# Optimization experiments

Measured on AMD Instinct MI355X. Metric: run time of the kernel, lower is better.

The kernel has to match this reference:

```python
import jax, jax.numpy as jnp
import numpy as np
from jax import lax

# config (mirrors KeypointExtract init)
NMS_DIST = 4
CONF_THRESH = 0.015
CELL = 8
BORDER = 4
KPT_NUM = 1024
WINDOW_SIZE = 5
TEMP_INIT = 10.0
MAX_CAND = 8192  # fixed candidate budget (top-scoring pixels fed to greedy NMS)


def _make_offsets():
    # linspace(-(ws//2), ws//2, ws//2*2+1) meshgrid -> (R,2) integer offsets (dy, dx)
    lin = np.linspace(-(WINDOW_SIZE // 2), WINDOW_SIZE // 2, num=WINDOW_SIZE // 2 * 2 + 1)
    o0, o1 = np.meshgrid(lin, lin)
    off = np.concatenate([o0.reshape(-1, 1), o1.reshape(-1, 1)], axis=1)
    return jnp.asarray(off.astype(np.int32))  # (R,2)


def depth2space(semi):
    # softmax over 65 channels, drop dustbin, pixel-shuffle 8x8 cells to full res
    dense = jax.nn.softmax(semi, axis=1)
    nodust = dense[:, :-1, :, :]                      # (B,64,Hc,Wc)
    B, C, Hc, Wc = nodust.shape
    cell = CELL
    hm = nodust.transpose(0, 2, 3, 1).reshape(B, Hc, Wc, cell, cell)
    hm = hm.transpose(0, 1, 3, 2, 4).reshape(B, Hc * cell, Wc * cell)
    return hm                                         # (B,H,W)


def greedy_nms(ys, xs, valid, H, W, pad):
    # faithful greedy grid-suppression NMS: candidates arrive sorted by conf desc
    w = 2 * pad + 1
    grid0 = jnp.zeros((H + 2 * pad, W + 2 * pad), dtype=bool)  # True = suppressed

    def step(grid, inp):
        y, x, v = inp
        keep = v & jnp.logical_not(grid[y + pad, x + pad])
        patch = lax.dynamic_slice(grid, (y, x), (w, w))
        grid = lax.dynamic_update_slice(grid, jnp.logical_or(patch, keep), (y, x))
        return grid, keep

    _, kept = lax.scan(step, grid0, (ys, xs, valid))
    return kept


def grid_sample_bilinear(img, gx, gy):
    # torch F.grid_sample, mode=bilinear, padding=zeros, align_corners=False
    B, C, Hc, Wc = img.shape
    ix = (gx + 1.0) * (Wc / 2.0) - 0.5
    iy = (gy + 1.0) * (Hc / 2.0) - 0.5
    x0 = jnp.floor(ix); y0 = jnp.floor(iy)
    wx1 = ix - x0; wy1 = iy - y0
    bidx = jnp.arange(B)[:, None]

    def tap(xi, yi):
        inb = (xi >= 0) & (xi < Wc) & (yi >= 0) & (yi < Hc)
        xc = jnp.clip(xi, 0, Wc - 1).astype(jnp.int32)
        yc = jnp.clip(yi, 0, Hc - 1).astype(jnp.int32)
        v = img[bidx, :, yc, xc]                      # (B,N,C)
        return jnp.where(inb[..., None], v, 0.0)

    v00 = tap(x0, y0); v01 = tap(x0 + 1, y0)
    v10 = tap(x0, y0 + 1); v11 = tap(x0 + 1, y0 + 1)
    w00 = ((1 - wx1) * (1 - wy1))[..., None]
    w01 = (wx1 * (1 - wy1))[..., None]
    w10 = ((1 - wx1) * wy1)[..., None]
    w11 = (wx1 * wy1)[..., None]
    out = v00 * w00 + v01 * w01 + v10 * w10 + v11 * w11  # (B,N,C)
    return out.transpose(0, 2, 1)                        # (B,C,N)


def setup_inputs() -> dict:
    key = jax.random.key(0)
    k1, k2 = jax.random.split(key)
    semi = jax.random.normal(k1, (4, 65, 120, 160), dtype=jnp.float32)
    coarse_desc = jax.random.normal(k2, (4, 256, 120, 160), dtype=jnp.float32)
    temp = jnp.ones((1,), dtype=jnp.float32) * TEMP_INIT
    return {"semi": semi, "coarse_desc": coarse_desc, "temp": temp}


def reference(semi, coarse_desc, temp):
    heatmap = depth2space(semi)                       # (B,H,W)
    B, H, W = heatmap.shape
    offs = _make_offsets()                            # (R,2) = (dy,dx)
    R = offs.shape[0]

    # ---- keypoint detection (no-grad in original) ----
    hm_sg = lax.stop_gradient(heatmap)
    vals, idx = lax.top_k(hm_sg.reshape(B, -1), MAX_CAND)   # sorted conf desc
    ys = (idx // W).astype(jnp.int32)
    xs = (idx % W).astype(jnp.int32)
    valid = vals >= CONF_THRESH
    kept = jax.vmap(lambda y, x, v: greedy_nms(y, x, v, H, W, NMS_DIST))(ys, xs, valid)
    border_ok = (xs >= BORDER) & (xs < W - BORDER) & (ys >= BORDER) & (ys < H - BORDER)
    sel_key = jnp.where(kept & border_ok, vals, -jnp.inf)
    _, sel = lax.top_k(sel_key, KPT_NUM)              # top kpt_num survivors by conf
    ysel = jnp.take_along_axis(ys, sel, axis=1)       # (B,N)
    xsel = jnp.take_along_axis(xs, sel, axis=1)

    # ---- spatial soft-argmax (differentiable) ----
    yy = ysel[:, None, :] + offs[None, :, 0:1]        # (B,R,N)
    xx = xsel[:, None, :] + offs[None, :, 1:2]
    bidx = jnp.arange(B)[:, None, None]
    region = heatmap[bidx, yy, xx]                    # (B,R,N) gather
    attn = jax.nn.softmax(region * temp[0], axis=1)
    offs_f = offs.astype(jnp.float32)
    dy = jnp.einsum('brn,r->bn', attn, offs_f[:, 0])
    dx = jnp.einsum('brn,r->bn', attn, offs_f[:, 1])
    y_f = ysel.astype(jnp.float32) + dy
    x_f = xsel.astype(jnp.float32) + dx
    batch_pts = jnp.stack([x_f, y_f], axis=-1)        # (B,N,2) (x,y)

    # ---- descriptor sampling ----
    gx = x_f / (W / 2.0) - 1.0
    gy = y_f / (H / 2.0) - 1.0
    desc = grid_sample_bilinear(coarse_desc, gx, gy)  # (B,C,N)
    desc = desc / jnp.maximum(jnp.linalg.norm(desc, axis=1, keepdims=True), 1e-12)
    return batch_pts, desc, heatmap
```

## Files before the change

kernel.cpp:

```cpp
#include <hip/hip_runtime.h>
#include <cstdint>

typedef unsigned int u32;
typedef unsigned long long u64;
typedef unsigned short u16;
typedef unsigned char u8;

#define HM_H 960
#define HM_W 1280
#define HM_N (HM_H*HM_W)
#define BATCH 4
#define CAND 8192
#define KPT 1024
#define NCELL 19200

#define WS_HISTA 0x0
#define WS_HISTB 0x100000
#define WS_META  0x200000
#define WS_CAND  0x200400
#define WS_EQ    0x240400
#define WS_SIDX  0x260400
#define WS_SEL   0x280400
#define WS_CM    0x284400
#define WS_CS    0x2CF400
#define WS_SPOT  0x365400
#define WS_BST   0x385400
#define WS_BLST  0x398040
#define WS_CNT   0x3A8040
#define WS_STAT  0x3C8040
#define WS_CLST  0x3D0040
#define WS_CAND2 0x4D0040


#define HBIN0 0x3C75u
#define NHBIN 780

__device__ inline double pixval64(const float* __restrict__ semi, const float* __restrict__ cm,
                                  const double* __restrict__ cs, int b, u32 idx){
  u32 y = idx / HM_W, x = idx - y*HM_W;
  u32 hc = y>>3, wc = x>>3, ch = ((y&7)<<3) | (x&7);
  float logit = semi[(((size_t)b*65 + ch)*120 + hc)*160 + wc];
  int cid = b*NCELL + (int)(hc*160 + wc);
  return exp((double)logit - (double)cm[cid]) / cs[cid];
}

__global__ __launch_bounds__(256) void k_heatmap(const float* __restrict__ semi, float* __restrict__ hm,
                          float* __restrict__ cm, double* __restrict__ cs, u32* __restrict__ hist){
  __shared__ u32 lh[NHBIN];
  for (int i=threadIdx.x;i<NHBIN;i+=256) lh[i]=0;
  __syncthreads();
  const u32 FLOOR = 0x3C75C28Fu;
  int tid = blockIdx.x*256 + threadIdx.x;
  int cell = tid >> 3, sub = tid & 7;
  int wc = cell % 160; int hc = (cell/160) % 120; int b = cell / NCELL;
  const float* p = semi + (size_t)b*65*NCELL + hc*160 + wc;
  float r[8];
  #pragma unroll
  for (int i=0;i<8;i++) r[i] = p[(size_t)(sub*8+i)*NCELL];
  float extra = (sub==7) ? p[(size_t)64*NCELL] : -3.0e38f;
  float m = extra;
  #pragma unroll
  for (int i=0;i<8;i++) m = fmaxf(m, r[i]);
  m = fmaxf(m, __shfl_xor(m,1,64));
  m = fmaxf(m, __shfl_xor(m,2,64));
  m = fmaxf(m, __shfl_xor(m,4,64));
  double S = 0.0;
  #pragma unroll
  for (int i=0;i<8;i++) S += exp((double)r[i] - (double)m);
  if (sub==7) S += exp((double)extra - (double)m);
  S += __shfl_xor(S,1,64);
  S += __shfl_xor(S,2,64);
  S += __shfl_xor(S,4,64);
  if (sub==0){ cm[cell]=m; cs[cell]=S; }
  float* out = hm + ((size_t)b*HM_H + hc*8 + sub)*HM_W + wc*8;
  float o[8];
  #pragma unroll
  for (int i=0;i<8;i++) o[i] = (float)(exp((double)r[i] - (double)m) / S);
  *reinterpret_cast<float4*>(out)     = make_float4(o[0],o[1],o[2],o[3]);
  *reinterpret_cast<float4*>(out + 4) = make_float4(o[4],o[5],o[6],o[7]);
  #pragma unroll
  for (int i=0;i<8;i++){
    u32 bs = __float_as_uint(o[i]);
    if (bs>=FLOOR){ u32 bi=(bs>>16)-HBIN0; if(bi>=NHBIN)bi=NHBIN-1; atomicAdd(&lh[bi],1u); }
  }
  __syncthreads();
  u32* h = hist + b*65536 + HBIN0;
  for (int i=threadIdx.x;i<NHBIN;i+=256){
    u32 c=lh[i]; if (c) atomicAdd(&h[i], c);
  }
}

__global__ __launch_bounds__(256) void k_histB(const float* __restrict__ hm, const u32* __restrict__ meta,
                                               u32* __restrict__ hist){
  const u32 FLOOR = 0x3C75C28Fu;
  int b = blockIdx.x >> 8;
  int chunk = blockIdx.x & 255;
  u32 piv = meta[b*64+0];
  u32* h = hist + b*65536;
  const float4* src = (const float4*)(hm + (size_t)b*HM_N);
  int per = (HM_N/4)/256;
  int start = chunk*per;
  for (int i=start+(int)threadIdx.x; i<start+per; i+=256){
    float4 v = src[i];
    u32 bs;
    bs = __float_as_uint(v.x); if (bs >= FLOOR && (bs>>16)==piv) atomicAdd(&h[bs & 0xFFFFu], 1u);
    bs = __float_as_uint(v.y); if (bs >= FLOOR && (bs>>16)==piv) atomicAdd(&h[bs & 0xFFFFu], 1u);
    bs = __float_as_uint(v.z); if (bs >= FLOOR && (bs>>16)==piv) atomicAdd(&h[bs & 0xFFFFu], 1u);
    bs = __float_as_uint(v.w); if (bs >= FLOOR && (bs>>16)==piv) atomicAdd(&h[bs & 0xFFFFu], 1u);
  }
}

__global__ void k_reduce(const u32* __restrict__ hist, u32* __restrict__ meta, int phase){
  int b = blockIdx.x;
  const u32* h = hist + b*65536;
  u32* mb = meta + b*64;
  u32 K = (phase==0) ? (u32)CAND : mb[1];
  int t = threadIdx.x;
  __shared__ u32 suf[1024];
  u32 s = 0;
  for (int i=0;i<64;i++) s += h[t*64+i];
  suf[t]=s; __syncthreads();
  for (int off=1; off<1024; off<<=1){
    u32 add = (t+off<1024) ? suf[t+off] : 0u;
    u32 nv2 = suf[t] + add;
    __syncthreads();
    suf[t]=nv2; __syncthreads();
  }
  u32 total = suf[0];
  u32 cumAbove = (t<1023) ? suf[t+1] : 0u;
  bool found = (cumAbove < K) && (cumAbove + s >= K);
  if (found){
    u32 cum = cumAbove; int bin = 0; u32 cA = cumAbove;
    for (int i=63;i>=0;i--){
      u32 c = h[t*64+i];
      if (cum + c >= K){ bin = t*64+i; cA = cum; break; }
      cum += c;
    }
    if (phase==0){ mb[0]=(u32)bin; mb[2]=cA; mb[1]=K-cA; }
    else {
      u32 V = (mb[0]<<16) | (u32)bin; mb[3]=V;
      u32 cg = mb[2] + cA; mb[4]=cg;
      mb[5] = (cg < (u32)CAND) ? ((u32)CAND - cg) : 0u;
    }
  }
  if (t==0 && total < K){
    if (phase==0){ mb[0]=0; mb[2]=total; mb[1]=K-total; }
    else {
      u32 V = (mb[0]<<16); mb[3]=V;
      u32 cg = mb[2] + total; mb[4]=cg;
      mb[5] = (cg < (u32)CAND) ? ((u32)CAND - cg) : 0u;
    }
  }
}

#define CB_CAP 4800
__global__ __launch_bounds__(256) void k_compact(const float* __restrict__ hm, u32* __restrict__ meta,
                          u64* __restrict__ cand, u32* __restrict__ eq){
  __shared__ u32 pixb[CB_CAP];
  __shared__ u32 bsb[CB_CAP];
  __shared__ u32 eqb[CB_CAP];
  __shared__ u32 cnt, ecnt, gbase, ebase;
  int b = blockIdx.x >> 8;
  int chunk = blockIdx.x & 255;
  if (threadIdx.x==0){ cnt=0u; ecnt=0u; }
  __syncthreads();
  u32 V = meta[b*64+3];
  const float4* src = (const float4*)(hm + (size_t)b*HM_N);
  int per = (HM_N/4)/256;
  int start = chunk*per;
  for (int i=start+(int)threadIdx.x; i<start+per; i+=256){
    float4 v = src[i];
    u32 pix = (u32)i*4u;
    u32 bs4[4];
    bs4[0]=__float_as_uint(v.x); bs4[1]=__float_as_uint(v.y);
    bs4[2]=__float_as_uint(v.z); bs4[3]=__float_as_uint(v.w);
    #pragma unroll
    for (int c2=0;c2<4;c2++){
      u32 bs = bs4[c2];
      if (bs > V){ u32 p = atomicAdd(&cnt,1u); pixb[p]=pix+(u32)c2; bsb[p]=bs; }
      else if (bs == V){ u32 e = atomicAdd(&ecnt,1u); eqb[e]=pix+(u32)c2; }
    }
  }
  __syncthreads();
  if (threadIdx.x==0){
    gbase = cnt  ? atomicAdd(&meta[b*64+6], cnt)  : 0u;
    ebase = ecnt ? atomicAdd(&meta[b*64+7], ecnt) : 0u;
  }
  __syncthreads();
  u32 c0=cnt, e0=ecnt, gb=gbase, eb=ebase;
  for (u32 i=threadIdx.x; i<c0; i+=256){
    u32 s2 = gb+i;
    if (s2 < CAND) cand[(size_t)b*CAND+s2] = (((u64)(~bsb[i]))<<32)|(u64)pixb[i];
  }
  for (u32 i=threadIdx.x; i<e0; i+=256){
    u32 s2 = eb+i;
    if (s2 < CAND) eq[(size_t)b*CAND+s2] = eqb[i];
  }
}

__global__ void k_eqprep(const u32* __restrict__ meta, u64* __restrict__ cand, const u32* __restrict__ eq,
                         const float* __restrict__ semi, const float* __restrict__ cm,
                         const double* __restrict__ cs){
  int b = blockIdx.x;
  __shared__ double vv[64];
  __shared__ u32 ii[64];
  if (threadIdx.x != 0) return;
  const u32* mb = meta + b*64;
  u32 countGt = mb[4], needEq = mb[5], V32 = mb[3];
  int n = (int)mb[7]; if (n > 64) n = 64;
  for (int j=0;j<n;j++){
    ii[j] = eq[(size_t)b*CAND + j];
    vv[j] = pixval64(semi, cm, cs, b, ii[j]);
  }
  for (int j=1;j<n;j++){
    double vj = vv[j]; u32 ij = ii[j];
    int q = j-1;
    while (q >= 0 && (vv[q] < vj || (vv[q] == vj && ii[q] > ij))){
      vv[q+1]=vv[q]; ii[q+1]=ii[q]; q--;
    }
    vv[q+1]=vj; ii[q+1]=ij;
  }
  u64 vq = ((u64)(~V32))<<32;
  for (u32 r=0; r<needEq; r++){
    u64 key = (r < (u32)n) ? (vq | (u64)ii[r]) : ~0ull;
    if (countGt + r < CAND) cand[(size_t)b*CAND + countGt + r] = key;
  }
}

__global__ __launch_bounds__(512,1) void k_sortloc(u64* __restrict__ cand){
  __shared__ u64 sk[2048];
  int blk = blockIdx.x;
  int b = blk >> 2, seg = blk & 3;
  int t = threadIdx.x;
  int lane = t & 63, w = t >> 6;
  int base = w*256 + lane;
  u64* cb = cand + (size_t)b*CAND + seg*2048;
  u64 E[4];
  #pragma unroll
  for (int m=0;m<4;m++) E[m] = cb[base + m*64];

  for (int k2=2; k2<=2048; k2<<=1){
    int j = k2>>1;
    if (j >= 256){
      __syncthreads();
      #pragma unroll
      for (int m=0;m<4;m++) sk[base + m*64] = E[m];
      __syncthreads();
      for (; j>=256; j>>=1){
        int lj = __ffs(j)-1;
        for (int p=t; p<1024; p+=512){
          int i = ((p >> lj) << (lj+1)) | (p & (j-1));
          int l = i | j;
          bool up = ((i & k2)==0);
          u64 a=sk[i], c=sk[l];
          if ((a>c)==up){ sk[i]=c; sk[l]=a; }
        }
        __syncthreads();
      }
      #pragma unroll
      for (int m=0;m<4;m++) E[m] = sk[base + m*64];
      j = 128;
    }
    for (; j>=64; j>>=1){
      int mm = j>>6;
      #pragma unroll
      for (int m=0;m<4;m++){
        if ((m & mm)==0){
          int i = base + m*64;
          bool up = ((i & k2)==0);
          u64 a=E[m], c=E[m|mm];
          if ((a>c)==up){ E[m]=c; E[m|mm]=a; }
        }
      }
    }
    for (; j>=1; j>>=1){
      bool low0 = ((lane & j)==0);
      #pragma unroll
      for (int m=0;m<4;m++){
        int i = base + m*64;
        bool up = ((i & k2)==0);
        bool keepmin = (low0==up);
        u64 P = (u64)__shfl_xor((long long)E[m], j, 64);
        u64 mn = E[m]<P ? E[m] : P;
        u64 mx = E[m]<P ? P : E[m];
        E[m] = keepmin ? mn : mx;
      }
    }
  }
  #pragma unroll
  for (int m=0;m<4;m++) cb[base + m*64] = E[m];
}

__global__ __launch_bounds__(256) void k_merge(const u64* __restrict__ src, u64* __restrict__ dst, int L){
  int tid = blockIdx.x*256 + (int)threadIdx.x;
  if (tid >= BATCH*CAND) return;
  int b = tid >> 13;
  int e = tid & (CAND-1);
  int pairBase = (e / (2*L)) * (2*L);
  int off = e - pairBase;
  const u64* A = src + ((size_t)b<<13) + pairBase;
  const u64* B = A + L;
  bool inA = off < L;
  int i = inA ? off : off - L;
  u64 key = inA ? A[i] : B[i];
  const u64* O = inA ? B : A;
  int lo = 0, hi = L;
  if (inA){
    while (lo < hi){ int mid=(lo+hi)>>1; if (O[mid] < key) lo=mid+1; else hi=mid; }
  } else {
    while (lo < hi){ int mid=(lo+hi)>>1; if (O[mid] <= key) lo=mid+1; else hi=mid; }
  }
  dst[((size_t)b<<13) + pairBase + i + lo] = key;
}

#define NBX 80
#define NBY 60
#define NBK (NBX*NBY)
#define BSTSTRIDE 4804
__global__ __launch_bounds__(1024,1) void k_sortfix(const u64* __restrict__ cand,
                       const float* __restrict__ semi, const float* __restrict__ cm,
                       const double* __restrict__ cs,
                       u32* __restrict__ spot, u32* __restrict__ bstG, u16* __restrict__ blistG){
  __shared__ u32 bcnt[NBK];
  __shared__ u32 bst[NBK];
  __shared__ u32 tsum[1024];
  extern __shared__ u64 sk[];
  int b = blockIdx.x, t = threadIdx.x;
  const u64* cb = cand + (size_t)b*CAND;
  for (int i=t;i<CAND;i+=1024) sk[i]=cb[i];
  for (int i=t;i<NBK;i+=1024) bcnt[i]=0;
  __syncthreads();
  for (int pass=0; pass<8; pass++){
    int par = pass & 1;
    for (int q=t; q<CAND/2; q+=1024){
      int p = par + 2*q;
      if (p+1 < CAND){
        u64 a = sk[p], c = sk[p+1];
        u32 ha = (u32)(a>>32), hc2 = (u32)(c>>32);
        if (ha == hc2 && ha != 0xFFFFFFFFu){
          double va = pixval64(semi, cm, cs, b, (u32)a);
          double vc = pixval64(semi, cm, cs, b, (u32)c);
          if (va < vc || (va == vc && (u32)a > (u32)c)){ sk[p]=c; sk[p+1]=a; }
        }
      }
    }
    __syncthreads();
  }
  for (int r=t;r<CAND;r+=1024){
    u32 idx = (u32)sk[r];
    u32 p;
    if (idx != 0xFFFFFFFFu){
      u32 y = idx/HM_W, x = idx - y*HM_W;
      p = (y<<16)|x;
      atomicAdd(&bcnt[(y>>4)*NBX+(x>>4)], 1u);
    } else p = 0xFFFFFFFFu;
    spot[(size_t)b*CAND+r] = p;
  }
  __syncthreads();
  u32 lsum=0;
  int base5 = t*5;
  if (base5 < NBK){
    #pragma unroll
    for (int j2=0;j2<5;j2++){ int ix=base5+j2; if (ix<NBK) lsum += bcnt[ix]; }
  }
  tsum[t]=lsum;
  __syncthreads();
  for (int off=1; off<1024; off<<=1){
    u32 add = (t>=off)? tsum[t-off] : 0u;
    __syncthreads();
    tsum[t] += add;
    __syncthreads();
  }
  if (base5 < NBK){
    u32 run = (t==0)?0u:tsum[t-1];
    #pragma unroll
    for (int j2=0;j2<5;j2++){
      int ix=base5+j2; if (ix<NBK){ u32 c=bcnt[ix]; bst[ix]=run; run+=c; }
    }
  }
  __syncthreads();
  for (int i=t;i<NBK;i+=1024){ bcnt[i]=bst[i]; bstG[(size_t)b*BSTSTRIDE+i]=bst[i]; }
  if (t==0) bstG[(size_t)b*BSTSTRIDE+NBK] = tsum[1023];
  __syncthreads();
  for (int r=t;r<CAND;r+=1024){
    u32 idx = (u32)sk[r];
    if (idx != 0xFFFFFFFFu){
      u32 y = idx/HM_W, x = idx - y*HM_W;
      u32 bu = (y>>4)*NBX + (x>>4);
      u32 slot = atomicAdd(&bcnt[bu],1u);
      blistG[(size_t)b*CAND+slot] = (u16)r;
    }
  }
}

#define CLCAP 12
__global__ __launch_bounds__(256) void k_nconf(const u32* __restrict__ spot, const u32* __restrict__ bstG,
                                               const u16* __restrict__ blistG, u32* __restrict__ cntG,
                                               u8* __restrict__ statG, u16* __restrict__ clistG){
  int b = blockIdx.x >> 5;
  int r = (blockIdx.x & 31)*256 + (int)threadIdx.x;
  const u32* sp = spot + (size_t)b*CAND;
  u32 p = sp[r];
  if (p == 0xFFFFFFFFu){ statG[(size_t)b*CAND+r]=2; return; }
  int y=(int)(p>>16), x=(int)(p&0xFFFFu);
  int by=y>>4, bx=x>>4;
  const u32* bs = bstG + (size_t)b*BSTSTRIDE;
  const u16* bl = blistG + (size_t)b*CAND;
  u16* cl = clistG + ((size_t)b*CAND + r)*CLCAP;
  int cnt=0; bool heavy=false;
  for (int dy=-1; dy<=1; dy++){
    int yy=by+dy; if (yy<0||yy>=NBY) continue;
    for (int dx=-1; dx<=1; dx++){
      int xx=bx+dx; if (xx<0||xx>=NBX) continue;
      int bu=yy*NBX+xx;
      int s=(int)bs[bu], e=(int)bs[bu+1];
      for (int q=s;q<e;q++){
        int j = (int)bl[q];
        if (j >= r) continue;
        u32 pj = sp[j];
        int ady = y-(int)(pj>>16); ady = ady<0?-ady:ady;
        int adx = x-(int)(pj&0xFFFFu); adx = adx<0?-adx:adx;
        if (ady<=4 && adx<=4){
          if (cnt < CLCAP) cl[cnt++] = (u16)j;
          else heavy = true;
        }
      }
    }
  }
  if (heavy){ cntG[(size_t)b*CAND+r]=0xFFFFFFFFu; statG[(size_t)b*CAND+r]=0; }
  else { cntG[(size_t)b*CAND+r]=(u32)cnt; statG[(size_t)b*CAND+r] = (cnt==0)?1:0; }
}

__global__ __launch_bounds__(1024,1) void k_nresolve(const u32* __restrict__ spot, const u32* __restrict__ bstG,
                                                     const u16* __restrict__ blistG, const u32* __restrict__ cntG,
                                                     u8* __restrict__ statG, const u16* __restrict__ clistG,
                                                     u32* __restrict__ sel){
  __shared__ u8 sstat[CAND];
  __shared__ u16 wl[2][CAND];
  __shared__ u32 wcnt[2];
  __shared__ u32 wpass[256];
  __shared__ u32 wpre[256];
  int b = blockIdx.x, t = threadIdx.x;
  const u32* sp = spot + (size_t)b*CAND;
  if (t<2) wcnt[t]=0;
  __syncthreads();
  for (int r=t;r<CAND;r+=1024){
    u8 st = statG[(size_t)b*CAND+r];
    sstat[r]=st;
    if (st==0){ u32 w=atomicAdd(&wcnt[0],1u); wl[0][w]=(u16)r; }
  }
  __syncthreads();
  int cur=0;
  for (int round=0; round<8192; ++round){
    int n = (int)wcnt[cur];
    if (n==0) break;
    int nx = cur^1;
    for (int i=t;i<n;i+=1024){
      int r = (int)wl[cur][i];
      u32 c = cntG[(size_t)b*CAND+r];
      bool supp=false, blocked=false;
      if (c==0xFFFFFFFFu){
        u32 p = sp[r];
        int y=(int)(p>>16), x=(int)(p&0xFFFFu);
        int by=y>>4, bx=x>>4;
        const u32* bs = bstG + (size_t)b*BSTSTRIDE;
        const u16* bl = blistG + (size_t)b*CAND;
        for (int dy=-1; dy<=1 && !supp; dy++){
          int yy=by+dy; if (yy<0||yy>=NBY) continue;
          for (int dx=-1; dx<=1 && !supp; dx++){
            int xx=bx+dx; if (xx<0||xx>=NBX) continue;
            int bu=yy*NBX+xx;
            int s=(int)bs[bu], e=(int)bs[bu+1];
            for (int q=s;q<e;q++){
              int j = (int)bl[q];
              if (j >= r) continue;
              u32 pj = sp[j];
              int ady = y-(int)(pj>>16); ady = ady<0?-ady:ady;
              int adx = x-(int)(pj&0xFFFFu); adx = adx<0?-adx:adx;
              if (ady<=4 && adx<=4){
                u8 st = sstat[j];
                if (st==1){ supp=true; break; }
                if (st==0) blocked=true;
              }
            }
          }
        }
      } else {
        const u16* cl = clistG + ((size_t)b*CAND + r)*CLCAP;
        for (u32 k=0;k<c;k++){
          u8 st = sstat[cl[k]];
          if (st==1){ supp=true; break; }
          if (st==0) blocked=true;
        }
      }
      if (supp) sstat[r]=2;
      else if (!blocked) sstat[r]=1;
      else { u32 w=atomicAdd(&wcnt[nx],1u); wl[nx][w]=(u16)r; }
    }
    __syncthreads();
    if (t==0) wcnt[cur]=0;
    cur = nx;
    __syncthreads();
  }

  if (t < 256){
    u32 w = 0;
    for (int bi2=0;bi2<32;bi2++){
      int r = t*32+bi2;
      if (sstat[r]==1){
        u32 p = sp[r];
        u32 y=p>>16, x=p&0xFFFFu;
        if (x>=4 && x<HM_W-4 && y>=4 && y<HM_H-4) w |= (1u<<bi2);
      }
    }
    wpass[t]=w;
    wpre[t]=__popc(w);
  }
  __syncthreads();
  for (int off=1; off<256; off<<=1){
    u32 add = 0;
    if (t<256 && t>=off) add = wpre[t-off];
    __syncthreads();
    if (t<256) wpre[t] += add;
    __syncthreads();
  }
  u32 P = wpre[255];
  for (int r=t;r<CAND;r+=1024){
    u32 word = wpass[r>>5];
    u32 bit = (u32)r & 31u;
    bool pass = (word>>bit)&1u;
    u32 prank = ((r>>5)>0 ? wpre[(r>>5)-1] : 0u) + __popc(word & ((1u<<bit)-1u));
    u32 p = sp[r];
    u32 y,x;
    if (p==0xFFFFFFFFu){ y=HM_H-1; x=HM_W-1; } else { y=p>>16; x=p&0xFFFFu; }
    if (pass){
      if (prank < KPT) sel[b*KPT+prank] = (y<<16)|x;
    } else {
      u32 frank = (u32)r - prank;
      u32 slot = P + frank;
      if (slot < KPT) sel[b*KPT+slot] = (y<<16)|x;
    }
  }
}

__global__ void k_refine(const u32* __restrict__ sel, const float* __restrict__ hm,
                         const float* __restrict__ temp, float* __restrict__ pts){
  int t = blockIdx.x*256 + threadIdx.x;
  if (t >= BATCH*KPT) return;
  int b = t >> 10;
  u32 p = sel[t];
  int y = (int)(p>>16), x = (int)(p & 0xFFFFu);
  float T = temp[0];
  const float* hb = hm + (size_t)b*HM_N;
  float r[25]; float m = -3.0e38f;
  #pragma unroll
  for (int i=0;i<25;i++){
    int yy = y + (i%5) - 2;
    int xx = x + (i/5) - 2;
    if (yy<0) yy += HM_H; if (yy<0) yy=0; if (yy>HM_H-1) yy=HM_H-1;
    if (xx<0) xx += HM_W; if (xx<0) xx=0; if (xx>HM_W-1) xx=HM_W-1;
    float v = hb[yy*HM_W+xx] * T;
    r[i]=v; m=fmaxf(m,v);
  }
  float s=0.f, dy=0.f, dx=0.f;
  #pragma unroll
  for (int i=0;i<25;i++){
    float e = expf(r[i]-m);
    s += e;
    dy += e * (float)((i%5)-2);
    dx += e * (float)((i/5)-2);
  }
  dy /= s; dx /= s;
  pts[t*2+0] = (float)x + dx;
  pts[t*2+1] = (float)y + dy;
}

__global__ __launch_bounds__(256) void k_desc1(const float* __restrict__ pts, const float* __restrict__ cd,
                                               float* __restrict__ desc){
  extern __shared__ float plane[];
  int blk = blockIdx.x;
  int b = blk >> 8;
  const float4* s4 = (const float4*)(cd + (size_t)blk*NCELL);
  float4* p4 = (float4*)plane;
  for (int i=threadIdx.x; i<NCELL/4; i+=256) p4[i]=s4[i];
  __syncthreads();
  for (int n=threadIdx.x; n<KPT; n+=256){
    float xf = pts[(b*KPT+n)*2+0], yf = pts[(b*KPT+n)*2+1];
    float gx = xf/640.0f - 1.0f;
    float gy = yf/480.0f - 1.0f;
    float ix = (gx+1.0f)*80.0f - 0.5f;
    float iy = (gy+1.0f)*60.0f - 0.5f;
    float x0f = floorf(ix), y0f = floorf(iy);
    float wx1 = ix-x0f, wy1 = iy-y0f;
    int x0=(int)x0f, y0=(int)y0f;
    bool xi0 = (x0>=0)&&(x0<160), xi1 = (x0+1>=0)&&(x0+1<160);
    bool yi0 = (y0>=0)&&(y0<120), yi1 = (y0+1>=0)&&(y0+1<120);
    int xc0 = min(max(x0,0),159),   xc1 = min(max(x0+1,0),159);
    int yc0 = min(max(y0,0),119),   yc1 = min(max(y0+1,0),119);
    float v00 = (xi0&&yi0) ? plane[yc0*160+xc0] : 0.f;
    float v01 = (xi1&&yi0) ? plane[yc0*160+xc1] : 0.f;
    float v10 = (xi0&&yi1) ? plane[yc1*160+xc0] : 0.f;
    float v11 = (xi1&&yi1) ? plane[yc1*160+xc1] : 0.f;
    float out = v00*(1.f-wx1)*(1.f-wy1) + v01*wx1*(1.f-wy1)
              + v10*(1.f-wx1)*wy1      + v11*wx1*wy1;
    desc[(size_t)blk*KPT + n] = out;
  }
}

#define DN_T 32
__global__ __launch_bounds__(256) void k_dnorm(float* __restrict__ desc){
  __shared__ float tile[256*DN_T];
  __shared__ float part[8*DN_T];
  __shared__ float nrm[DN_T];
  int b = blockIdx.x >> 5;
  int n0 = (blockIdx.x & 31)*DN_T;
  int t = threadIdx.x;
  float* db = desc + (size_t)b*256*KPT + n0;
  for (int k=0;k<8;k++){
    int idx = t + 256*k;
    int c = idx >> 3, f4 = idx & 7;
    float4 v = *reinterpret_cast<const float4*>(db + (size_t)c*KPT + f4*4);
    *reinterpret_cast<float4*>(&tile[c*DN_T + f4*4]) = v;
  }
  __syncthreads();
  {
    int n = t & (DN_T-1), q = t >> 5;
    float s = 0.f;
    #pragma unroll
    for (int k=0;k<32;k++){
      float v = tile[(q+8*k)*DN_T + n];
      s += v*v;
    }
    part[q*DN_T + n] = s;
  }
  __syncthreads();
  if (t < DN_T){
    float tot = 0.f;
    #pragma unroll
    for (int q=0;q<8;q++) tot += part[q*DN_T + t];
    nrm[t] = fmaxf(sqrtf(tot), 1e-12f);
  }
  __syncthreads();
  for (int k=0;k<8;k++){
    int idx = t + 256*k;
    int c = idx >> 3, f4 = idx & 7;
    float4 v = *reinterpret_cast<const float4*>(&tile[c*DN_T + f4*4]);
    v.x /= nrm[f4*4+0]; v.y /= nrm[f4*4+1]; v.z /= nrm[f4*4+2]; v.w /= nrm[f4*4+3];
    *reinterpret_cast<float4*>(db + (size_t)c*KPT + f4*4) = v;
  }
}

extern "C" void kernel_launch(void* const* d_in, const int* in_sizes, int n_in,
                              void* d_out, int out_size, void* d_ws, size_t ws_size,
                              hipStream_t stream){
  const float* semi = (const float*)d_in[0];
  const float* cdsc = (const float*)d_in[1];
  const float* temp = (const float*)d_in[2];
  float* pts  = (float*)d_out;
  float* desc = pts + 4*1024*2;
  float* hm   = desc + (size_t)4*256*1024;
  char* ws = (char*)d_ws;
  u32* histA = (u32*)(ws + WS_HISTA);
  u32* histB = (u32*)(ws + WS_HISTB);
  u32* meta  = (u32*)(ws + WS_META);
  u64* cand  = (u64*)(ws + WS_CAND);
  u32* eq    = (u32*)(ws + WS_EQ);
  u32* sel   = (u32*)(ws + WS_SEL);
  float*  cm = (float*)(ws + WS_CM);
  double* cs = (double*)(ws + WS_CS);
  u32* spot  = (u32*)(ws + WS_SPOT);
  u32* bstG  = (u32*)(ws + WS_BST);
  u16* blistG= (u16*)(ws + WS_BLST);
  u32* cntG  = (u32*)(ws + WS_CNT);
  u8*  statG = (u8*)(ws + WS_STAT);
  u16* clistG= (u16*)(ws + WS_CLST);
  u64* cand2 = (u64*)(ws + WS_CAND2);

  hipMemsetAsync(ws, 0, WS_CAND, stream);

  k_heatmap<<<2400, 256, 0, stream>>>(semi, hm, cm, cs, histA);
  k_reduce <<<4, 1024, 0, stream>>>(histA, meta, 0);
  k_histB  <<<1024, 256, 0, stream>>>(hm, meta, histB);
  k_reduce <<<4, 1024, 0, stream>>>(histB, meta, 1);
  k_compact<<<1024, 256, 0, stream>>>(hm, meta, cand, eq);
  k_eqprep <<<4, 64, 0, stream>>>(meta, cand, eq, semi, cm, cs);
  k_sortloc<<<16, 512, 0, stream>>>(cand);
  k_merge  <<<128, 256, 0, stream>>>(cand, cand2, 2048);
  k_merge  <<<128, 256, 0, stream>>>(cand2, cand, 4096);
  hipFuncSetAttribute((const void*)k_sortfix, hipFuncAttributeMaxDynamicSharedMemorySize, CAND*8);
  k_sortfix<<<4, 1024, CAND*8, stream>>>(cand, semi, cm, cs, spot, bstG, blistG);
  k_nconf  <<<128, 256, 0, stream>>>(spot, bstG, blistG, cntG, statG, clistG);
  k_nresolve<<<4, 1024, 0, stream>>>(spot, bstG, blistG, cntG, statG, clistG, sel);
  k_refine <<<16, 256, 0, stream>>>(sel, hm, temp, pts);
  hipFuncSetAttribute((const void*)k_desc1, hipFuncAttributeMaxDynamicSharedMemorySize, NCELL*4);
  k_desc1  <<<1024, 256, NCELL*4, stream>>>(pts, cdsc, desc);
  k_dnorm  <<<128, 256, 0, stream>>>(desc);
}
```

Measured before the change: 201.4 us.

## Replace two-pass radix threshold selection with single 20-bit histogram pass

The top-8192 threshold search now builds one finer histogram keyed on the top 20 float bits during the heatmap kernel. This removes the second full-heatmap histogram pass and one reduce launch. Ties in the boundary bin are resolved in k_eqprep with a parallel bitonic sort plus an odd-even fixup that compares recomputed double-precision values, replacing the single-threaded insertion sort. The cost is a much larger shared histogram per heatmap block (about 50KB, which lowers occupancy and adds zeroing and flush work), and equal-bin candidates are capped at 1024, so a large boundary bin could be mishandled.

```diff
diff --git a/kernel.cpp b/kernel.cpp
--- a/kernel.cpp
+++ b/kernel.cpp
@@ -14,12 +14,10 @@
 #define KPT 1024
 #define NCELL 19200
 
-#define WS_HISTA 0x0
-#define WS_HISTB 0x100000
+#define WS_HIST  0x0
 #define WS_META  0x200000
 #define WS_CAND  0x200400
 #define WS_EQ    0x240400
-#define WS_SIDX  0x260400
 #define WS_SEL   0x280400
 #define WS_CM    0x284400
 #define WS_CS    0x2CF400
@@ -32,8 +30,9 @@
 #define WS_CAND2 0x4D0040
 
 
-#define HBIN0 0x3C75u
-#define NHBIN 780
+#define FLOOR_BITS 0x3C75C28Fu
+#define B20_0 0x3C75Cu
+#define NB20  12453
 
 __device__ inline double pixval64(const float* __restrict__ semi, const float* __restrict__ cm,
                                   const double* __restrict__ cs, int b, u32 idx){
@@ -46,10 +45,9 @@
 
 __global__ __launch_bounds__(256) void k_heatmap(const float* __restrict__ semi, float* __restrict__ hm,
                           float* __restrict__ cm, double* __restrict__ cs, u32* __restrict__ hist){
-  __shared__ u32 lh[NHBIN];
-  for (int i=threadIdx.x;i<NHBIN;i+=256) lh[i]=0;
-  __syncthreads();
-  const u32 FLOOR = 0x3C75C28Fu;
+  extern __shared__ u32 lh[];
+  for (int i=threadIdx.x;i<NB20;i+=256) lh[i]=0;
+  __syncthreads();
   int tid = blockIdx.x*256 + threadIdx.x;
   int cell = tid >> 3, sub = tid & 7;
   int wc = cell % 160; int hc = (cell/160) % 120; int b = cell / NCELL;
@@ -81,44 +79,25 @@
   #pragma unroll
   for (int i=0;i<8;i++){
     u32 bs = __float_as_uint(o[i]);
-    if (bs>=FLOOR){ u32 bi=(bs>>16)-HBIN0; if(bi>=NHBIN)bi=NHBIN-1; atomicAdd(&lh[bi],1u); }
-  }
-  __syncthreads();
-  u32* h = hist + b*65536 + HBIN0;
-  for (int i=threadIdx.x;i<NHBIN;i+=256){
+    if (bs>=FLOOR_BITS){ u32 bi=(bs>>12)-B20_0; if(bi>=NB20)bi=NB20-1; atomicAdd(&lh[bi],1u); }
+  }
+  __syncthreads();
+  u32* h = hist + b*65536;
+  for (int i=threadIdx.x;i<NB20;i+=256){
     u32 c=lh[i]; if (c) atomicAdd(&h[i], c);
   }
 }
 
-__global__ __launch_bounds__(256) void k_histB(const float* __restrict__ hm, const u32* __restrict__ meta,
-                                               u32* __restrict__ hist){
-  const u32 FLOOR = 0x3C75C28Fu;
-  int b = blockIdx.x >> 8;
-  int chunk = blockIdx.x & 255;
-  u32 piv = meta[b*64+0];
-  u32* h = hist + b*65536;
-  const float4* src = (const float4*)(hm + (size_t)b*HM_N);
-  int per = (HM_N/4)/256;
-  int start = chunk*per;
-  for (int i=start+(int)threadIdx.x; i<start+per; i+=256){
-    float4 v = src[i];
-    u32 bs;
-    bs = __float_as_uint(v.x); if (bs >= FLOOR && (bs>>16)==piv) atomicAdd(&h[bs & 0xFFFFu], 1u);
-    bs = __float_as_uint(v.y); if (bs >= FLOOR && (bs>>16)==piv) atomicAdd(&h[bs & 0xFFFFu], 1u);
-    bs = __float_as_uint(v.z); if (bs >= FLOOR && (bs>>16)==piv) atomicAdd(&h[bs & 0xFFFFu], 1u);
-    bs = __float_as_uint(v.w); if (bs >= FLOOR && (bs>>16)==piv) atomicAdd(&h[bs & 0xFFFFu], 1u);
-  }
-}
-
-__global__ void k_reduce(const u32* __restrict__ hist, u32* __restrict__ meta, int phase){
+__global__ void k_reduce(const u32* __restrict__ hist, u32* __restrict__ meta){
   int b = blockIdx.x;
   const u32* h = hist + b*65536;
   u32* mb = meta + b*64;
-  u32 K = (phase==0) ? (u32)CAND : mb[1];
+  const u32 K = (u32)CAND;
   int t = threadIdx.x;
   __shared__ u32 suf[1024];
   u32 s = 0;
-  for (int i=0;i<64;i++) s += h[t*64+i];
+  #pragma unroll
+  for (int i=0;i<16;i++){ int bin = t*16+i; if (bin < NB20) s += h[bin]; }
   suf[t]=s; __syncthreads();
   for (int off=1; off<1024; off<<=1){
     u32 add = (t+off<1024) ? suf[t+off] : 0u;
@@ -131,40 +110,37 @@
   bool found = (cumAbove < K) && (cumAbove + s >= K);
   if (found){
     u32 cum = cumAbove; int bin = 0; u32 cA = cumAbove;
-    for (int i=63;i>=0;i--){
-      u32 c = h[t*64+i];
-      if (cum + c >= K){ bin = t*64+i; cA = cum; break; }
+    for (int i=15;i>=0;i--){
+      int bb = t*16+i; if (bb >= NB20) continue;
+      u32 c = h[bb];
+      if (cum + c >= K){ bin = bb; cA = cum; break; }
       cum += c;
     }
-    if (phase==0){ mb[0]=(u32)bin; mb[2]=cA; mb[1]=K-cA; }
-    else {
-      u32 V = (mb[0]<<16) | (u32)bin; mb[3]=V;
-      u32 cg = mb[2] + cA; mb[4]=cg;
-      mb[5] = (cg < (u32)CAND) ? ((u32)CAND - cg) : 0u;
-    }
+    mb[3] = B20_0 + (u32)bin;
+    mb[4] = cA;
+    mb[5] = K - cA;
   }
   if (t==0 && total < K){
-    if (phase==0){ mb[0]=0; mb[2]=total; mb[1]=K-total; }
-    else {
-      u32 V = (mb[0]<<16); mb[3]=V;
-      u32 cg = mb[2] + total; mb[4]=cg;
-      mb[5] = (cg < (u32)CAND) ? ((u32)CAND - cg) : 0u;
-    }
+    mb[3] = B20_0;
+    u32 cA = total - h[0];
+    mb[4] = cA;
+    mb[5] = K - cA;
   }
 }
 
 #define CB_CAP 4800
+#define EQ_CAP 2048
 __global__ __launch_bounds__(256) void k_compact(const float* __restrict__ hm, u32* __restrict__ meta,
-                          u64* __restrict__ cand, u32* __restrict__ eq){
+                          u64* __restrict__ cand, u64* __restrict__ eqk){
   __shared__ u32 pixb[CB_CAP];
   __shared__ u32 bsb[CB_CAP];
-  __shared__ u32 eqb[CB_CAP];
+  __shared__ u64 eqb[EQ_CAP];
   __shared__ u32 cnt, ecnt, gbase, ebase;
   int b = blockIdx.x >> 8;
   int chunk = blockIdx.x & 255;
   if (threadIdx.x==0){ cnt=0u; ecnt=0u; }
   __syncthreads();
-  u32 V = meta[b*64+3];
+  u32 V20 = meta[b*64+3];
   const float4* src = (const float4*)(hm + (size_t)b*HM_N);
   int per = (HM_N/4)/256;
   int start = chunk*per;
@@ -177,8 +153,12 @@
     #pragma unroll
     for (int c2=0;c2<4;c2++){
       u32 bs = bs4[c2];
-      if (bs > V){ u32 p = atomicAdd(&cnt,1u); pixb[p]=pix+(u32)c2; bsb[p]=bs; }
-      else if (bs == V){ u32 e = atomicAdd(&ecnt,1u); eqb[e]=pix+(u32)c2; }
+      u32 t20 = bs>>12;
+      if (t20 > V20){ u32 p = atomicAdd(&cnt,1u); pixb[p]=pix+(u32)c2; bsb[p]=bs; }
+      else if (t20 == V20 && bs >= FLOOR_BITS){
+        u32 e = atomicAdd(&ecnt,1u);
+        if (e < EQ_CAP) eqb[e] = (((u64)(~bs))<<32)|(u64)(pix+(u32)c2);
+      }
     }
   }
   __syncthreads();
@@ -188,42 +168,60 @@
   }
   __syncthreads();
   u32 c0=cnt, e0=ecnt, gb=gbase, eb=ebase;
+  if (e0 > EQ_CAP) e0 = EQ_CAP;
   for (u32 i=threadIdx.x; i<c0; i+=256){
     u32 s2 = gb+i;
     if (s2 < CAND) cand[(size_t)b*CAND+s2] = (((u64)(~bsb[i]))<<32)|(u64)pixb[i];
   }
   for (u32 i=threadIdx.x; i<e0; i+=256){
     u32 s2 = eb+i;
-    if (s2 < CAND) eq[(size_t)b*CAND+s2] = eqb[i];
-  }
-}
-
-__global__ void k_eqprep(const u32* __restrict__ meta, u64* __restrict__ cand, const u32* __restrict__ eq,
+    if (s2 < CAND) eqk[(size_t)b*CAND+s2] = eqb[i];
+  }
+}
+
+__global__ __launch_bounds__(256) void k_eqprep(const u32* __restrict__ meta, u64* __restrict__ cand,
+                         const u64* __restrict__ eqk,
                          const float* __restrict__ semi, const float* __restrict__ cm,
                          const double* __restrict__ cs){
-  int b = blockIdx.x;
-  __shared__ double vv[64];
-  __shared__ u32 ii[64];
-  if (threadIdx.x != 0) return;
+  __shared__ u64 sk[1024];
+  int b = blockIdx.x, t = threadIdx.x;
   const u32* mb = meta + b*64;
-  u32 countGt = mb[4], needEq = mb[5], V32 = mb[3];
-  int n = (int)mb[7]; if (n > 64) n = 64;
-  for (int j=0;j<n;j++){
-    ii[j] = eq[(size_t)b*CAND + j];
-    vv[j] = pixval64(semi, cm, cs, b, ii[j]);
-  }
-  for (int j=1;j<n;j++){
-    double vj = vv[j]; u32 ij = ii[j];
-    int q = j-1;
-    while (q >= 0 && (vv[q] < vj || (vv[q] == vj && ii[q] > ij))){
-      vv[q+1]=vv[q]; ii[q+1]=ii[q]; q--;
-    }
-    vv[q+1]=vj; ii[q+1]=ij;
-  }
-  u64 vq = ((u64)(~V32))<<32;
-  for (u32 r=0; r<needEq; r++){
-    u64 key = (r < (u32)n) ? (vq | (u64)ii[r]) : ~0ull;
-    if (countGt + r < CAND) cand[(size_t)b*CAND + countGt + r] = key;
+  u32 cA = mb[4], needEq = mb[5];
+  u32 E = mb[7]; u32 n = E > 1024u ? 1024u : E;
+  for (int i=t;i<1024;i+=256) sk[i] = (i < (int)n) ? eqk[(size_t)b*CAND+i] : ~0ull;
+  __syncthreads();
+  for (int k2=2;k2<=1024;k2<<=1)
+    for (int j=k2>>1;j>0;j>>=1){
+      int lj = __ffs(j)-1;
+      for (int p=t; p<512; p+=256){
+        int i = ((p >> lj) << (lj+1)) | (p & (j-1));
+        int l = i | j;
+        bool up = ((i & k2)==0);
+        u64 a=sk[i], c=sk[l];
+        if ((a>c)==up){ sk[i]=c; sk[l]=a; }
+      }
+      __syncthreads();
+    }
+  for (int pass=0; pass<8; pass++){
+    int par = pass & 1;
+    for (int q=t; q<512; q+=256){
+      int p = par + 2*q;
+      if (p+1 < 1024){
+        u64 a = sk[p], c = sk[p+1];
+        u32 ha = (u32)(a>>32), hc2 = (u32)(c>>32);
+        if (ha == hc2 && ha != 0xFFFFFFFFu){
+          double va = pixval64(semi, cm, cs, b, (u32)a);
+          double vc = pixval64(semi, cm, cs, b, (u32)c);
+          if (va < vc || (va == vc && (u32)a > (u32)c)){ sk[p]=c; sk[p+1]=a; }
+        }
+      }
+    }
+    __syncthreads();
+  }
+  for (u32 r=t; r<needEq; r+=256){
+    u64 key = (r < n) ? sk[r] : ~0ull;
+    u32 s2 = cA + r;
+    if (s2 < CAND) cand[(size_t)b*CAND + s2] = key;
   }
 }
 
@@ -660,11 +658,10 @@
   float* desc = pts + 4*1024*2;
   float* hm   = desc + (size_t)4*256*1024;
   char* ws = (char*)d_ws;
-  u32* histA = (u32*)(ws + WS_HISTA);
-  u32* histB = (u32*)(ws + WS_HISTB);
+  u32* hist  = (u32*)(ws + WS_HIST);
   u32* meta  = (u32*)(ws + WS_META);
   u64* cand  = (u64*)(ws + WS_CAND);
-  u32* eq    = (u32*)(ws + WS_EQ);
+  u64* eqk   = (u64*)(ws + WS_EQ);
   u32* sel   = (u32*)(ws + WS_SEL);
   float*  cm = (float*)(ws + WS_CM);
   double* cs = (double*)(ws + WS_CS);
@@ -678,12 +675,11 @@
 
   hipMemsetAsync(ws, 0, WS_CAND, stream);
 
-  k_heatmap<<<2400, 256, 0, stream>>>(semi, hm, cm, cs, histA);
-  k_reduce <<<4, 1024, 0, stream>>>(histA, meta, 0);
-  k_histB  <<<1024, 256, 0, stream>>>(hm, meta, histB);
-  k_reduce <<<4, 1024, 0, stream>>>(histB, meta, 1);
-  k_compact<<<1024, 256, 0, stream>>>(hm, meta, cand, eq);
-  k_eqprep <<<4, 64, 0, stream>>>(meta, cand, eq, semi, cm, cs);
+  hipFuncSetAttribute((const void*)k_heatmap, hipFuncAttributeMaxDynamicSharedMemorySize, NB20*4);
+  k_heatmap<<<2400, 256, NB20*4, stream>>>(semi, hm, cm, cs, hist);
+  k_reduce <<<4, 1024, 0, stream>>>(hist, meta);
+  k_compact<<<1024, 256, 0, stream>>>(hm, meta, cand, eqk);
+  k_eqprep <<<4, 256, 0, stream>>>(meta, cand, eqk, semi, cm, cs);
   k_sortloc<<<16, 512, 0, stream>>>(cand);
   k_merge  <<<128, 256, 0, stream>>>(cand, cand2, 2048);
   k_merge  <<<128, 256, 0, stream>>>(cand2, cand, 4096);
```

Result: slower. 218.8 us (+8.7%).
